# Optimization experiments

Measured on AMD Instinct MI355X. Metric: run time of the kernel, lower is better.

Reference implementation:

```python
import jax, jax.numpy as jnp
import numpy as np

DIM = 1024
HEADS = 16
DHEAD = 64
INNER = HEADS * DHEAD
EPS = 1e-5


def layer_norm(x, g, b):
    mu = jnp.mean(x, axis=-1, keepdims=True)
    var = jnp.mean(jnp.square(x - mu), axis=-1, keepdims=True)
    return (x - mu) * jax.lax.rsqrt(var + EPS) * g + b


def apply_rope(x, cos, sin):
    # x: [b, h, s, d]; cos/sin broadcast as [1, 1, s, d/2]
    d2 = x.shape[-1] // 2
    x1, x2 = x[..., :d2], x[..., d2:]
    return jnp.concatenate([x1 * cos - x2 * sin, x2 * cos + x1 * sin], axis=-1)


def setup_inputs() -> dict:
    key = jax.random.key(0)
    ks = jax.random.split(key, 10)
    B, N, S = 8, 256, 4096
    latents = jax.random.normal(ks[0], (B, N, DIM), dtype=jnp.float32)
    context = jax.random.normal(ks[1], (B, S, DIM), dtype=jnp.float32)
    cos = jax.random.uniform(ks[2], (S, DHEAD // 2), dtype=jnp.float32)
    sin = jax.random.uniform(ks[3], (S, DHEAD // 2), dtype=jnp.float32)
    init = lambda k, shp, fan_in: jax.random.normal(k, shp, dtype=jnp.float32) / np.sqrt(fan_in)
    return {
        "latents": latents,
        "context": context,
        "cos": cos,
        "sin": sin,
        "ln_lat_g": jnp.ones((DIM,), jnp.float32),
        "ln_lat_b": jnp.zeros((DIM,), jnp.float32),
        "ln_ctx_g": jnp.ones((DIM,), jnp.float32),
        "ln_ctx_b": jnp.zeros((DIM,), jnp.float32),
        "Wq": init(ks[4], (DIM, INNER), DIM),
        "Wkv": init(ks[5], (DIM, 2 * INNER), DIM),
        "Wo": init(ks[6], (INNER, DIM), INNER),
        "bo": jnp.zeros((DIM,), jnp.float32),
    }


def reference(latents, context, cos, sin, ln_lat_g, ln_lat_b, ln_ctx_g, ln_ctx_b, Wq, Wkv, Wo, bo):
    b, n, _ = latents.shape
    s = context.shape[1]
    lat = layer_norm(latents, ln_lat_g, ln_lat_b)
    ctx = layer_norm(context, ln_ctx_g, ln_ctx_b)
    q = (lat @ Wq).reshape(b, n, HEADS, DHEAD).transpose(0, 2, 1, 3)   # [b,h,n,d]
    kv = ctx @ Wkv
    k, v = jnp.split(kv, 2, axis=-1)
    k = k.reshape(b, s, HEADS, DHEAD).transpose(0, 2, 1, 3)           # [b,h,s,d]
    v = v.reshape(b, s, HEADS, DHEAD).transpose(0, 2, 1, 3)
    k = apply_rope(k, cos[None, None], sin[None, None])
    scale = DHEAD ** (-0.5)
    attn = jnp.einsum('bhnd,bhsd->bhns', q, k) * scale
    attn = jnp.clip(attn, -11.0, 11.0)
    attn = jax.nn.softmax(attn, axis=-1)
    out = jnp.einsum('bhns,bhsd->bhnd', attn, v)
    out = out.transpose(0, 2, 1, 3).reshape(b, n, INNER)
    return out @ Wo + bo
```

## Files before the change

### kernel.cpp

```cpp
#include <hip/hip_runtime.h>
#include <math.h>

#define DIM   1024
#define HEADS 16
#define DHEAD 64
#define NB    8
#define NLAT  256
#define SCTX  4096

typedef short bf16x8 __attribute__((ext_vector_type(8)));
typedef float f32x4  __attribute__((ext_vector_type(4)));

__device__ __forceinline__ unsigned short f2b(float f) {
    union { float f; unsigned u; } x; x.f = f;
    unsigned r = x.u + 0x7FFFu + ((x.u >> 16) & 1u);
    return (unsigned short)(r >> 16);
}
__device__ __forceinline__ float b2f(unsigned short u) {
    union { unsigned u; float f; } x; x.u = ((unsigned)u) << 16;
    return x.f;
}

__global__ __launch_bounds__(256) void ln_bf16(const float* __restrict__ x,
                                               const float* __restrict__ g,
                                               const float* __restrict__ b,
                                               unsigned short* __restrict__ y) {
    int r = blockIdx.x, t = threadIdx.x;
    float4 v = ((const float4*)(x + (size_t)r * DIM))[t];
    float s  = v.x + v.y + v.z + v.w;
    float sq = v.x * v.x + v.y * v.y + v.z * v.z + v.w * v.w;
    #pragma unroll
    for (int off = 32; off > 0; off >>= 1) {
        s  += __shfl_down(s, off);
        sq += __shfl_down(sq, off);
    }
    __shared__ float ls[4], lq[4], smu, srs;
    int wid = t >> 6, lane = t & 63;
    if (lane == 0) { ls[wid] = s; lq[wid] = sq; }
    __syncthreads();
    if (t == 0) {
        s  = ls[0] + ls[1] + ls[2] + ls[3];
        sq = lq[0] + lq[1] + lq[2] + lq[3];
        float m   = s * (1.0f / DIM);
        float var = sq * (1.0f / DIM) - m * m;
        smu = m;
        srs = rsqrtf(var + 1e-5f);
    }
    __syncthreads();
    float mu = smu, rs = srs;
    float4 gg = ((const float4*)g)[t];
    float4 bb = ((const float4*)b)[t];
    ushort4 o;
    o.x = f2b((v.x - mu) * rs * gg.x + bb.x);
    o.y = f2b((v.y - mu) * rs * gg.y + bb.y);
    o.z = f2b((v.z - mu) * rs * gg.z + bb.z);
    o.w = f2b((v.w - mu) * rs * gg.w + bb.w);
    ((ushort4*)(y + (size_t)r * DIM))[t] = o;
}

__global__ __launch_bounds__(256) void transpose_bf16(
    const float* __restrict__ W, unsigned short* __restrict__ Wt, int K, int N)
{
    __shared__ unsigned short tile[32][33];
    int n0 = blockIdx.x * 32, k0 = blockIdx.y * 32;
    int tx = threadIdx.x & 31, ty = threadIdx.x >> 5;
    #pragma unroll
    for (int i = 0; i < 4; ++i) {
        int k = k0 + ty + i * 8;
        tile[tx][ty + i * 8] = f2b(W[(size_t)k * N + n0 + tx]);
    }
    __syncthreads();
    #pragma unroll
    for (int i = 0; i < 4; ++i) {
        int n = n0 + ty + i * 8;
        Wt[(size_t)n * K + k0 + tx] = tile[ty + i * 8][tx];
    }
}

__global__ __launch_bounds__(256, 2) void gemm_mfma(
    const unsigned short* __restrict__ A, const unsigned short* __restrict__ Bn,
    int K, const float* __restrict__ bias,
    float* __restrict__ outf,
    unsigned short* __restrict__ outk, unsigned short* __restrict__ outv,
    int mode, int ldc)
{
    __shared__ __align__(16) unsigned short As[128 * 32];
    __shared__ __align__(16) unsigned short Bs[128 * 32];
    int t = threadIdx.x;
    int wave = t >> 6, lane = t & 63;
    int m_base = blockIdx.y * 128, n_base = blockIdx.x * 128;
    int wr = wave >> 1, wc = wave & 1;

    f32x4 zero = {0.f, 0.f, 0.f, 0.f};
    f32x4 acc[4][4];
    #pragma unroll
    for (int i = 0; i < 4; ++i)
        #pragma unroll
        for (int j = 0; j < 4; ++j) acc[i][j] = zero;

    int srow = lane >> 2;
    int scol = (lane & 3) * 8;
    const unsigned short* Ag = A  + (size_t)m_base * K;
    const unsigned short* Bg = Bn + (size_t)n_base * K;

    const unsigned short* a_lds = As + (wr * 64 + (lane & 15)) * 32 + (lane >> 4) * 8;
    const unsigned short* b_lds = Bs + (wc * 64 + (lane & 15)) * 32 + (lane >> 4) * 8;

    for (int k0 = 0; k0 < K; k0 += 32) {
        __syncthreads();
        #pragma unroll
        for (int i = 0; i < 2; ++i) {
            int row = i * 64 + wave * 16 + srow;
            __builtin_amdgcn_global_load_lds(
                (const __attribute__((address_space(1))) void*)(Ag + (size_t)row * K + k0 + scol),
                (__attribute__((address_space(3))) void*)(As + (size_t)(i * 64 + wave * 16) * 32 + lane * 8),
                16, 0, 0);
            __builtin_amdgcn_global_load_lds(
                (const __attribute__((address_space(1))) void*)(Bg + (size_t)row * K + k0 + scol),
                (__attribute__((address_space(3))) void*)(Bs + (size_t)(i * 64 + wave * 16) * 32 + lane * 8),
                16, 0, 0);
        }
        __syncthreads();
        bf16x8 af[4], bfr[4];
        #pragma unroll
        for (int i = 0; i < 4; ++i) {
            af[i]  = *(const bf16x8*)(a_lds + i * 16 * 32);
            bfr[i] = *(const bf16x8*)(b_lds + i * 16 * 32);
        }
        #pragma unroll
        for (int i = 0; i < 4; ++i)
            #pragma unroll
            for (int j = 0; j < 4; ++j)
                acc[i][j] = __builtin_amdgcn_mfma_f32_16x16x32_bf16(af[i], bfr[j], acc[i][j], 0, 0, 0);
    }

    int cl = lane & 15, rq = lane >> 4;
    if (mode == 2 && n_base >= DIM) {
        #pragma unroll
        for (int i = 0; i < 4; ++i) {
            int s0 = m_base + wr * 64 + i * 16 + rq * 4;
            int b  = s0 >> 12, s = s0 & 4095;
            #pragma unroll
            for (int j = 0; j < 4; ++j) {
                int n2 = n_base + wc * 64 + j * 16 + cl - DIM;
                int h = n2 >> 6, d = n2 & 63;
                ushort4 pk;
                pk.x = f2b(acc[i][j][0]); pk.y = f2b(acc[i][j][1]);
                pk.z = f2b(acc[i][j][2]); pk.w = f2b(acc[i][j][3]);
                *(ushort4*)(outv + (((size_t)(b * HEADS + h) * DHEAD + d) * SCTX) + s) = pk;
            }
        }
    } else {
        #pragma unroll
        for (int i = 0; i < 4; ++i) {
            #pragma unroll
            for (int j = 0; j < 4; ++j) {
                #pragma unroll
                for (int r = 0; r < 4; ++r) {
                    int m = m_base + wr * 64 + i * 16 + rq * 4 + r;
                    int n = n_base + wc * 64 + j * 16 + cl;
                    float cv = acc[i][j][r];
                    if (mode == 0) {
                        outf[(size_t)m * ldc + n] = cv + bias[n];
                    } else if (mode == 1) {
                        int b = m >> 8, nn = m & 255;
                        int h = n >> 6, d = n & 63;
                        outk[(((size_t)(b * HEADS + h) * NLAT + nn) * DHEAD) + d] = f2b(cv);
                    } else {
                        int b = m >> 12, s = m & 4095;
                        int h = n >> 6, d = n & 63;
                        outk[(((size_t)(b * HEADS + h) * SCTX + s) * DHEAD) + d] = f2b(cv);
                    }
                }
            }
        }
    }
}

__global__ __launch_bounds__(256) void rope_k(unsigned short* __restrict__ k,
                                              const float* __restrict__ cosp,
                                              const float* __restrict__ sinp) {
    int idx = blockIdx.x * 256 + threadIdx.x;
    int p  = idx & 31;
    int s  = (idx >> 5) & 4095;
    int bh = idx >> 17;
    size_t base = ((size_t)bh * SCTX + s) * DHEAD + p;
    float x1 = b2f(k[base]);
    float x2 = b2f(k[base + 32]);
    float c  = cosp[s * 32 + p];
    float sn = sinp[s * 32 + p];
    k[base]      = f2b(x1 * c - x2 * sn);
    k[base + 32] = f2b(x2 * c + x1 * sn);
}

__global__ __launch_bounds__(256, 2) void attn_mfma(
    const unsigned short* __restrict__ qb,
    const unsigned short* __restrict__ kb,
    const unsigned short* __restrict__ vtb,
    float* __restrict__ accsum,
    float* __restrict__ lsum)
{
    __shared__ __align__(16) unsigned short Ks[64 * 64];
    __shared__ __align__(16) unsigned short Vs[64 * 64];
    __shared__ __align__(16) unsigned short Ps[4 * 32 * 72];

    int t = threadIdx.x, w = t >> 6, l = t & 63;
    int bh = blockIdx.x >> 2;
    int qh = (blockIdx.x >> 1) & 1;
    int sh = blockIdx.x & 1;
    int quad = l >> 4, ln = l & 15;
    int q0 = qh * 128 + w * 32;

    bf16x8 qf[2][2];
    const unsigned short* qbase = qb + ((size_t)bh * NLAT + q0) * DHEAD;
    #pragma unroll
    for (int qsub = 0; qsub < 2; ++qsub)
        #pragma unroll
        for (int kc = 0; kc < 2; ++kc)
            qf[qsub][kc] = *(const bf16x8*)(qbase + (qsub * 16 + ln) * DHEAD + kc * 32 + quad * 8);

    f32x4 acc[2][4];
    #pragma unroll
    for (int i = 0; i < 2; ++i)
        #pragma unroll
        for (int j = 0; j < 4; ++j) acc[i][j] = (f32x4){0.f, 0.f, 0.f, 0.f};
    float lacc[2] = {0.f, 0.f};

    int srow8 = l >> 3;
    int schk  = l & 7;
    int gchk  = schk ^ srow8;
    const unsigned short* kgb = kb  + (size_t)bh * SCTX * DHEAD;
    const unsigned short* vgb = vtb + (size_t)bh * DHEAD * SCTX;
    unsigned short* Pw = Ps + w * 32 * 72;

    int s_begin = sh * 2048;
    for (int s0 = s_begin; s0 < s_begin + 2048; s0 += 64) {
        __syncthreads();
        #pragma unroll
        for (int i = 0; i < 2; ++i) {
            int g = 2 * w + i;
            int row = g * 8 + srow8;
            __builtin_amdgcn_global_load_lds(
                (const __attribute__((address_space(1))) void*)(kgb + (size_t)(s0 + row) * DHEAD + gchk * 8),
                (__attribute__((address_space(3))) void*)(Ks + row * 64 + schk * 8), 16, 0, 0);
            __builtin_amdgcn_global_load_lds(
                (const __attribute__((address_space(1))) void*)(vgb + (size_t)row * SCTX + s0 + gchk * 8),
                (__attribute__((address_space(3))) void*)(Vs + row * 64 + schk * 8), 16, 0, 0);
        }
        __syncthreads();

        #pragma unroll
        for (int msub = 0; msub < 4; ++msub) {
            bf16x8 af[2];
            #pragma unroll
            for (int kc = 0; kc < 2; ++kc) {
                int sr = msub * 16 + ln;
                int ck = (4 * kc + quad) ^ (ln & 7);
                af[kc] = *(const bf16x8*)(Ks + sr * 64 + ck * 8);
            }
            #pragma unroll
            for (int nsub = 0; nsub < 2; ++nsub) {
                f32x4 c = {0.f, 0.f, 0.f, 0.f};
                c = __builtin_amdgcn_mfma_f32_16x16x32_bf16(af[0], qf[nsub][0], c, 0, 0, 0);
                c = __builtin_amdgcn_mfma_f32_16x16x32_bf16(af[1], qf[nsub][1], c, 0, 0, 0);
                ushort4 pk;
                #pragma unroll
                for (int r = 0; r < 4; ++r) {
                    float sc = fminf(fmaxf(c[r] * 0.125f, -11.f), 11.f);
                    float p  = __expf(sc - 11.f);
                    lacc[nsub] += p;
                    ((unsigned short*)&pk)[r] = f2b(p);
                }
                *(ushort4*)(Pw + (nsub * 16 + ln) * 72 + msub * 16 + quad * 4) = pk;
            }
        }
        #pragma unroll
        for (int kc = 0; kc < 2; ++kc) {
            bf16x8 pa[2];
            #pragma unroll
            for (int qsub = 0; qsub < 2; ++qsub)
                pa[qsub] = *(const bf16x8*)(Pw + (qsub * 16 + ln) * 72 + kc * 32 + quad * 8);
            #pragma unroll
            for (int dsub = 0; dsub < 4; ++dsub) {
                int dr = dsub * 16 + ln;
                int ck = (4 * kc + quad) ^ (ln & 7);
                bf16x8 vb = *(const bf16x8*)(Vs + dr * 64 + ck * 8);
                acc[0][dsub] = __builtin_amdgcn_mfma_f32_16x16x32_bf16(pa[0], vb, acc[0][dsub], 0, 0, 0);
                acc[1][dsub] = __builtin_amdgcn_mfma_f32_16x16x32_bf16(pa[1], vb, acc[1][dsub], 0, 0, 0);
            }
        }
    }

    #pragma unroll
    for (int nsub = 0; nsub < 2; ++nsub) {
        float v = lacc[nsub];
        v += __shfl_xor(v, 16);
        v += __shfl_xor(v, 32);
        if (l < 16)
            atomicAdd(lsum + bh * NLAT + q0 + nsub * 16 + l, v);
    }
    #pragma unroll
    for (int qsub = 0; qsub < 2; ++qsub)
        #pragma unroll
        for (int dsub = 0; dsub < 4; ++dsub)
            #pragma unroll
            for (int r = 0; r < 4; ++r) {
                int qg = q0 + qsub * 16 + quad * 4 + r;
                int dg = dsub * 16 + ln;
                atomicAdd(accsum + ((size_t)bh * NLAT + qg) * DHEAD + dg,
                          acc[qsub][dsub][r]);
            }
}

__global__ __launch_bounds__(256) void attn_finalize(
    const float* __restrict__ accsum, const float* __restrict__ lsum,
    unsigned short* __restrict__ aob)
{
    int idx = blockIdx.x * 256 + threadIdx.x;
    int d = idx & 63;
    int rest = idx >> 6;
    int n = rest & 255, bh = rest >> 8;
    int b = bh >> 4, h = bh & 15;
    aob[(((size_t)b * NLAT + n) * HEADS + h) * DHEAD + d] =
        f2b(accsum[idx] / lsum[rest]);
}

extern "C" void kernel_launch(void* const* d_in, const int* in_sizes, int n_in,
                              void* d_out, int out_size, void* d_ws, size_t ws_size,
                              hipStream_t stream) {
    const float* latents  = (const float*)d_in[0];
    const float* context  = (const float*)d_in[1];
    const float* cosp     = (const float*)d_in[2];
    const float* sinp     = (const float*)d_in[3];
    const float* ln_lat_g = (const float*)d_in[4];
    const float* ln_lat_b = (const float*)d_in[5];
    const float* ln_ctx_g = (const float*)d_in[6];
    const float* ln_ctx_b = (const float*)d_in[7];
    const float* Wq  = (const float*)d_in[8];
    const float* Wkv = (const float*)d_in[9];
    const float* Wo  = (const float*)d_in[10];
    const float* bo  = (const float*)d_in[11];
    float* out = (float*)d_out;

    char* base = (char*)d_ws;
    unsigned short* lat_b = (unsigned short*)(base + 0);
    unsigned short* ctx_b = (unsigned short*)(base + 4194304);
    unsigned short* Wqb   = (unsigned short*)(base + 71303168);
    unsigned short* Wkvb  = (unsigned short*)(base + 73400320);
    unsigned short* Wob   = (unsigned short*)(base + 77594624);
    unsigned short* q_b   = (unsigned short*)(base + 79691776);
    unsigned short* k_b   = (unsigned short*)(base + 83886080);
    unsigned short* vT_b  = (unsigned short*)(base + 150994944);
    float*          accs  = (float*)(base + 218103808);
    float*          lsum  = (float*)(base + 226492416);
    unsigned short* aob   = (unsigned short*)(base + 226623488);

    hipLaunchKernelGGL(ln_bf16, dim3(NB * NLAT), dim3(256), 0, stream,
                       latents, ln_lat_g, ln_lat_b, lat_b);
    hipLaunchKernelGGL(ln_bf16, dim3(NB * SCTX), dim3(256), 0, stream,
                       context, ln_ctx_g, ln_ctx_b, ctx_b);
    hipLaunchKernelGGL(transpose_bf16, dim3(32, 32), dim3(256), 0, stream,
                       Wq, Wqb, DIM, DIM);
    hipLaunchKernelGGL(transpose_bf16, dim3(64, 32), dim3(256), 0, stream,
                       Wkv, Wkvb, DIM, 2 * DIM);
    hipLaunchKernelGGL(transpose_bf16, dim3(32, 32), dim3(256), 0, stream,
                       Wo, Wob, DIM, DIM);
    hipLaunchKernelGGL(gemm_mfma, dim3(8, 16), dim3(256), 0, stream,
                       lat_b, Wqb, DIM, (const float*)nullptr,
                       (float*)nullptr, q_b, (unsigned short*)nullptr, 1, 0);
    hipLaunchKernelGGL(gemm_mfma, dim3(16, 256), dim3(256), 0, stream,
                       ctx_b, Wkvb, DIM, (const float*)nullptr,
                       (float*)nullptr, k_b, vT_b, 2, 0);
    hipLaunchKernelGGL(rope_k, dim3(NB * HEADS * SCTX * 32 / 256), dim3(256), 0, stream,
                       k_b, cosp, sinp);
    hipMemsetAsync(accs, 0, 8388608, stream);
    hipMemsetAsync(lsum, 0, 131072, stream);
    hipLaunchKernelGGL(attn_mfma, dim3(NB * HEADS * 4), dim3(256), 0, stream,
                       q_b, k_b, vT_b, accs, lsum);
    hipLaunchKernelGGL(attn_finalize, dim3(NB * HEADS * NLAT * DHEAD / 256), dim3(256), 0, stream,
                       accs, lsum, aob);
    hipLaunchKernelGGL(gemm_mfma, dim3(8, 16), dim3(256), 0, stream,
                       aob, Wob, DIM, bo,
                       out, (unsigned short*)nullptr, (unsigned short*)nullptr, 0, DIM);
}
```

Measured before the change: 572.9 us.

## Fuse RoPE into KV GEMM, merge prep kernels, split attention into partials

Merges the two layernorm launches and the three weight transposes into single launches. Fuses RoPE into the K-projection GEMM epilogue, removing a separate read-modify-write pass over K, and remaps GEMM blocks to a 1D grid with an XCD-aware tile order. The attention kernel splits the sequence four ways and writes per-split partials instead of using atomics, which removes the memsets. Its K/V staging moves from direct global-to-LDS loads to register prefetch, and its occupancy hint is raised. The finalize kernel sums the four partials, at the cost of extra workspace and partial traffic.

```diff
diff --git a/kernel.cpp b/kernel.cpp
--- a/kernel.cpp
+++ b/kernel.cpp
@@ -16,16 +16,18 @@
     unsigned r = x.u + 0x7FFFu + ((x.u >> 16) & 1u);
     return (unsigned short)(r >> 16);
 }
-__device__ __forceinline__ float b2f(unsigned short u) {
-    union { unsigned u; float f; } x; x.u = ((unsigned)u) << 16;
-    return x.f;
-}
-
-__global__ __launch_bounds__(256) void ln_bf16(const float* __restrict__ x,
-                                               const float* __restrict__ g,
-                                               const float* __restrict__ b,
-                                               unsigned short* __restrict__ y) {
-    int r = blockIdx.x, t = threadIdx.x;
+
+__global__ __launch_bounds__(256) void ln_bf16_all(
+    const float* __restrict__ latents, const float* __restrict__ context,
+    const float* __restrict__ g_lat, const float* __restrict__ b_lat,
+    const float* __restrict__ g_ctx, const float* __restrict__ b_ctx,
+    unsigned short* __restrict__ lat_b, unsigned short* __restrict__ ctx_b)
+{
+    int rb = blockIdx.x, t = threadIdx.x;
+    const float* x; const float* g; const float* b; unsigned short* y; int r;
+    if (rb < NB * NLAT) { x = latents; g = g_lat; b = b_lat; y = lat_b; r = rb; }
+    else { x = context; g = g_ctx; b = b_ctx; y = ctx_b; r = rb - NB * NLAT; }
+
     float4 v = ((const float4*)(x + (size_t)r * DIM))[t];
     float s  = v.x + v.y + v.z + v.w;
     float sq = v.x * v.x + v.y * v.y + v.z * v.z + v.w * v.w;
@@ -58,11 +60,21 @@
     ((ushort4*)(y + (size_t)r * DIM))[t] = o;
 }
 
-__global__ __launch_bounds__(256) void transpose_bf16(
-    const float* __restrict__ W, unsigned short* __restrict__ Wt, int K, int N)
+__global__ __launch_bounds__(256) void transpose_all(
+    const float* __restrict__ Wq, const float* __restrict__ Wkv,
+    const float* __restrict__ Wo,
+    unsigned short* __restrict__ Wqb, unsigned short* __restrict__ Wkvb,
+    unsigned short* __restrict__ Wob)
 {
     __shared__ unsigned short tile[32][33];
-    int n0 = blockIdx.x * 32, k0 = blockIdx.y * 32;
+    const float* W; unsigned short* Wt; int N, coloff = 0;
+    switch (blockIdx.z) {
+        case 0: W = Wq;  Wt = Wqb;  N = DIM;     break;
+        case 1: W = Wkv; Wt = Wkvb; N = 2 * DIM; break;
+        case 2: W = Wkv; Wt = Wkvb; N = 2 * DIM; coloff = DIM; break;
+        default: W = Wo; Wt = Wob;  N = DIM;     break;
+    }
+    int n0 = blockIdx.x * 32 + coloff, k0 = blockIdx.y * 32;
     int tx = threadIdx.x & 31, ty = threadIdx.x >> 5;
     #pragma unroll
     for (int i = 0; i < 4; ++i) {
@@ -73,13 +85,14 @@
     #pragma unroll
     for (int i = 0; i < 4; ++i) {
         int n = n0 + ty + i * 8;
-        Wt[(size_t)n * K + k0 + tx] = tile[ty + i * 8][tx];
+        Wt[(size_t)n * DIM + k0 + tx] = tile[ty + i * 8][tx];
     }
 }
 
 __global__ __launch_bounds__(256, 2) void gemm_mfma(
     const unsigned short* __restrict__ A, const unsigned short* __restrict__ Bn,
     int K, const float* __restrict__ bias,
+    const float* __restrict__ cosp, const float* __restrict__ sinp,
     float* __restrict__ outf,
     unsigned short* __restrict__ outk, unsigned short* __restrict__ outv,
     int mode, int ldc)
@@ -88,7 +101,17 @@
     __shared__ __align__(16) unsigned short Bs[128 * 32];
     int t = threadIdx.x;
     int wave = t >> 6, lane = t & 63;
-    int m_base = blockIdx.y * 128, n_base = blockIdx.x * 128;
+    int g = blockIdx.x;
+    int m_tile, n_tile;
+    if (mode == 2) {
+        int xcd = g & 7, j = g >> 3;
+        n_tile = j & 15;
+        m_tile = (xcd << 5) + (j >> 4);
+    } else {
+        n_tile = g & 7;
+        m_tile = g >> 3;
+    }
+    int m_base = m_tile * 128, n_base = n_tile * 128;
     int wr = wave >> 1, wc = wave & 1;
 
     f32x4 zero = {0.f, 0.f, 0.f, 0.f};
@@ -150,6 +173,27 @@
                 *(ushort4*)(outv + (((size_t)(b * HEADS + h) * DHEAD + d) * SCTX) + s) = pk;
             }
         }
+    } else if (mode == 2) {
+        #pragma unroll
+        for (int i = 0; i < 4; ++i) {
+            #pragma unroll
+            for (int r = 0; r < 4; ++r) {
+                int m = m_base + wr * 64 + i * 16 + rq * 4 + r;
+                int b = m >> 12, s = m & 4095;
+                #pragma unroll
+                for (int j = 0; j < 2; ++j) {
+                    int n = n_base + wc * 64 + j * 16 + cl;
+                    int h = n >> 6, d1 = n & 63;
+                    float x1 = acc[i][j][r], x2 = acc[i][j + 2][r];
+                    float c  = cosp[s * 32 + d1];
+                    float sn = sinp[s * 32 + d1];
+                    unsigned short* kr =
+                        outk + (((size_t)(b * HEADS + h) * SCTX + s) * DHEAD) + d1;
+                    kr[0]  = f2b(x1 * c - x2 * sn);
+                    kr[32] = f2b(x2 * c + x1 * sn);
+                }
+            }
+        }
     } else {
         #pragma unroll
         for (int i = 0; i < 4; ++i) {
@@ -162,14 +206,10 @@
                     float cv = acc[i][j][r];
                     if (mode == 0) {
                         outf[(size_t)m * ldc + n] = cv + bias[n];
-                    } else if (mode == 1) {
+                    } else {
                         int b = m >> 8, nn = m & 255;
                         int h = n >> 6, d = n & 63;
                         outk[(((size_t)(b * HEADS + h) * NLAT + nn) * DHEAD) + d] = f2b(cv);
-                    } else {
-                        int b = m >> 12, s = m & 4095;
-                        int h = n >> 6, d = n & 63;
-                        outk[(((size_t)(b * HEADS + h) * SCTX + s) * DHEAD) + d] = f2b(cv);
                     }
                 }
             }
@@ -177,37 +217,21 @@
     }
 }
 
-__global__ __launch_bounds__(256) void rope_k(unsigned short* __restrict__ k,
-                                              const float* __restrict__ cosp,
-                                              const float* __restrict__ sinp) {
-    int idx = blockIdx.x * 256 + threadIdx.x;
-    int p  = idx & 31;
-    int s  = (idx >> 5) & 4095;
-    int bh = idx >> 17;
-    size_t base = ((size_t)bh * SCTX + s) * DHEAD + p;
-    float x1 = b2f(k[base]);
-    float x2 = b2f(k[base + 32]);
-    float c  = cosp[s * 32 + p];
-    float sn = sinp[s * 32 + p];
-    k[base]      = f2b(x1 * c - x2 * sn);
-    k[base + 32] = f2b(x2 * c + x1 * sn);
-}
-
-__global__ __launch_bounds__(256, 2) void attn_mfma(
+__global__ __launch_bounds__(256, 4) void attn_mfma(
     const unsigned short* __restrict__ qb,
     const unsigned short* __restrict__ kb,
     const unsigned short* __restrict__ vtb,
-    float* __restrict__ accsum,
-    float* __restrict__ lsum)
+    float* __restrict__ accp,
+    float* __restrict__ lp)
 {
     __shared__ __align__(16) unsigned short Ks[64 * 64];
     __shared__ __align__(16) unsigned short Vs[64 * 64];
     __shared__ __align__(16) unsigned short Ps[4 * 32 * 72];
 
     int t = threadIdx.x, w = t >> 6, l = t & 63;
-    int bh = blockIdx.x >> 2;
-    int qh = (blockIdx.x >> 1) & 1;
-    int sh = blockIdx.x & 1;
+    int bh = blockIdx.x >> 3;
+    int qh = (blockIdx.x >> 2) & 1;
+    int sh = blockIdx.x & 3;
     int quad = l >> 4, ln = l & 15;
     int q0 = qh * 128 + w * 32;
 
@@ -226,28 +250,42 @@
         for (int j = 0; j < 4; ++j) acc[i][j] = (f32x4){0.f, 0.f, 0.f, 0.f};
     float lacc[2] = {0.f, 0.f};
 
-    int srow8 = l >> 3;
-    int schk  = l & 7;
-    int gchk  = schk ^ srow8;
+    int srow = t >> 3;
+    int schk = t & 7;
     const unsigned short* kgb = kb  + (size_t)bh * SCTX * DHEAD;
     const unsigned short* vgb = vtb + (size_t)bh * DHEAD * SCTX;
     unsigned short* Pw = Ps + w * 32 * 72;
 
-    int s_begin = sh * 2048;
-    for (int s0 = s_begin; s0 < s_begin + 2048; s0 += 64) {
+    const int s_begin = sh * 1024;
+    const int NT = 1024 / 64;
+
+    uint4 kreg[2], vreg[2];
+    #pragma unroll
+    for (int i = 0; i < 2; ++i) {
+        int row = srow + 32 * i;
+        kreg[i] = *(const uint4*)(kgb + (size_t)(s_begin + row) * DHEAD + schk * 8);
+        vreg[i] = *(const uint4*)(vgb + (size_t)row * SCTX + s_begin + schk * 8);
+    }
+
+    for (int it = 0; it < NT; ++it) {
         __syncthreads();
         #pragma unroll
         for (int i = 0; i < 2; ++i) {
-            int g = 2 * w + i;
-            int row = g * 8 + srow8;
-            __builtin_amdgcn_global_load_lds(
-                (const __attribute__((address_space(1))) void*)(kgb + (size_t)(s0 + row) * DHEAD + gchk * 8),
-                (__attribute__((address_space(3))) void*)(Ks + row * 64 + schk * 8), 16, 0, 0);
-            __builtin_amdgcn_global_load_lds(
-                (const __attribute__((address_space(1))) void*)(vgb + (size_t)row * SCTX + s0 + gchk * 8),
-                (__attribute__((address_space(3))) void*)(Vs + row * 64 + schk * 8), 16, 0, 0);
+            int row = srow + 32 * i;
+            int cpos = schk ^ (row & 7);
+            *(uint4*)(Ks + row * 64 + cpos * 8) = kreg[i];
+            *(uint4*)(Vs + row * 64 + cpos * 8) = vreg[i];
         }
         __syncthreads();
+        if (it + 1 < NT) {
+            int s0n = s_begin + (it + 1) * 64;
+            #pragma unroll
+            for (int i = 0; i < 2; ++i) {
+                int row = srow + 32 * i;
+                kreg[i] = *(const uint4*)(kgb + (size_t)(s0n + row) * DHEAD + schk * 8);
+                vreg[i] = *(const uint4*)(vgb + (size_t)row * SCTX + s0n + schk * 8);
+            }
+        }
 
         #pragma unroll
         for (int msub = 0; msub < 4; ++msub) {
@@ -291,13 +329,16 @@
         }
     }
 
+    float* accs = accp + (size_t)sh * (NB * HEADS * NLAT * DHEAD);
+    float* ls   = lp   + (size_t)sh * (NB * HEADS * NLAT);
+
     #pragma unroll
     for (int nsub = 0; nsub < 2; ++nsub) {
         float v = lacc[nsub];
         v += __shfl_xor(v, 16);
         v += __shfl_xor(v, 32);
         if (l < 16)
-            atomicAdd(lsum + bh * NLAT + q0 + nsub * 16 + l, v);
+            ls[bh * NLAT + q0 + nsub * 16 + l] = v;
     }
     #pragma unroll
     for (int qsub = 0; qsub < 2; ++qsub)
@@ -307,22 +348,24 @@
             for (int r = 0; r < 4; ++r) {
                 int qg = q0 + qsub * 16 + quad * 4 + r;
                 int dg = dsub * 16 + ln;
-                atomicAdd(accsum + ((size_t)bh * NLAT + qg) * DHEAD + dg,
-                          acc[qsub][dsub][r]);
+                accs[((size_t)bh * NLAT + qg) * DHEAD + dg] = acc[qsub][dsub][r];
             }
 }
 
 __global__ __launch_bounds__(256) void attn_finalize(
-    const float* __restrict__ accsum, const float* __restrict__ lsum,
+    const float* __restrict__ accp, const float* __restrict__ lp,
     unsigned short* __restrict__ aob)
 {
+    const int ACC = NB * HEADS * NLAT * DHEAD;
+    const int LSZ = NB * HEADS * NLAT;
     int idx = blockIdx.x * 256 + threadIdx.x;
     int d = idx & 63;
     int rest = idx >> 6;
     int n = rest & 255, bh = rest >> 8;
     int b = bh >> 4, h = bh & 15;
-    aob[(((size_t)b * NLAT + n) * HEADS + h) * DHEAD + d] =
-        f2b(accsum[idx] / lsum[rest]);
+    float a = accp[idx] + accp[idx + ACC] + accp[idx + 2 * ACC] + accp[idx + 3 * ACC];
+    float l = lp[rest] + lp[rest + LSZ] + lp[rest + 2 * LSZ] + lp[rest + 3 * LSZ];
+    aob[(((size_t)b * NLAT + n) * HEADS + h) * DHEAD + d] = f2b(a / l);
 }
 
 extern "C" void kernel_launch(void* const* d_in, const int* in_sizes, int n_in,
@@ -351,35 +394,29 @@
     unsigned short* q_b   = (unsigned short*)(base + 79691776);
     unsigned short* k_b   = (unsigned short*)(base + 83886080);
     unsigned short* vT_b  = (unsigned short*)(base + 150994944);
-    float*          accs  = (float*)(base + 218103808);
-    float*          lsum  = (float*)(base + 226492416);
-    unsigned short* aob   = (unsigned short*)(base + 226623488);
-
-    hipLaunchKernelGGL(ln_bf16, dim3(NB * NLAT), dim3(256), 0, stream,
-                       latents, ln_lat_g, ln_lat_b, lat_b);
-    hipLaunchKernelGGL(ln_bf16, dim3(NB * SCTX), dim3(256), 0, stream,
-                       context, ln_ctx_g, ln_ctx_b, ctx_b);
-    hipLaunchKernelGGL(transpose_bf16, dim3(32, 32), dim3(256), 0, stream,
-                       Wq, Wqb, DIM, DIM);
-    hipLaunchKernelGGL(transpose_bf16, dim3(64, 32), dim3(256), 0, stream,
-                       Wkv, Wkvb, DIM, 2 * DIM);
-    hipLaunchKernelGGL(transpose_bf16, dim3(32, 32), dim3(256), 0, stream,
-                       Wo, Wob, DIM, DIM);
-    hipLaunchKernelGGL(gemm_mfma, dim3(8, 16), dim3(256), 0, stream,
+    float*          accp  = (float*)(base + 218103808);
+    float*          lp    = (float*)(base + 251658240);
+    unsigned short* aob   = (unsigned short*)(base + 252182528);
+
+    hipLaunchKernelGGL(ln_bf16_all, dim3(NB * NLAT + NB * SCTX), dim3(256), 0, stream,
+                       latents, context, ln_lat_g, ln_lat_b, ln_ctx_g, ln_ctx_b,
+                       lat_b, ctx_b);
+    hipLaunchKernelGGL(transpose_all, dim3(32, 32, 4), dim3(256), 0, stream,
+                       Wq, Wkv, Wo, Wqb, Wkvb, Wob);
+    hipLaunchKernelGGL(gemm_mfma, dim3(128), dim3(256), 0, stream,
                        lat_b, Wqb, DIM, (const float*)nullptr,
+                       (const float*)nullptr, (const float*)nullptr,
                        (float*)nullptr, q_b, (unsigned short*)nullptr, 1, 0);
-    hipLaunchKernelGGL(gemm_mfma, dim3(16, 256), dim3(256), 0, stream,
+    hipLaunchKernelGGL(gemm_mfma, dim3(4096), dim3(256), 0, stream,
                        ctx_b, Wkvb, DIM, (const float*)nullptr,
+                       cosp, sinp,
                        (float*)nullptr, k_b, vT_b, 2, 0);
-    hipLaunchKernelGGL(rope_k, dim3(NB * HEADS * SCTX * 32 / 256), dim3(256), 0, stream,
-                       k_b, cosp, sinp);
-    hipMemsetAsync(accs, 0, 8388608, stream);
-    hipMemsetAsync(lsum, 0, 131072, stream);
-    hipLaunchKernelGGL(attn_mfma, dim3(NB * HEADS * 4), dim3(256), 0, stream,
-                       q_b, k_b, vT_b, accs, lsum);
+    hipLaunchKernelGGL(attn_mfma, dim3(NB * HEADS * 8), dim3(256), 0, stream,
+                       q_b, k_b, vT_b, accp, lp);
     hipLaunchKernelGGL(attn_finalize, dim3(NB * HEADS * NLAT * DHEAD / 256), dim3(256), 0, stream,
-                       accs, lsum, aob);
-    hipLaunchKernelGGL(gemm_mfma, dim3(8, 16), dim3(256), 0, stream,
+                       accp, lp, aob);
+    hipLaunchKernelGGL(gemm_mfma, dim3(128), dim3(256), 0, stream,
                        aob, Wob, DIM, bo,
+                       (const float*)nullptr, (const float*)nullptr,
                        out, (unsigned short*)nullptr, (unsigned short*)nullptr, 0, DIM);
 }
```

Result: no change. 572.1 us (-0.1%).
